# Kernel tuning notes

Hardware: AMD Instinct MI355X
Metric: run time of the kernel (lower is better)

Reference implementation:

```python
import jax, jax.numpy as jnp
import numpy as np

B, CIN, COUT, CLEV = 1, 128, 128, 64
H, W = 48, 160            # height//2**scale, width//2**scale (scale=2)
MIN_D, MAX_D = 0.1, 100.0


def conv3x3(x, w, b, mode):
    x = jnp.pad(x, ((0, 0), (0, 0), (1, 1), (1, 1)), mode=mode)
    y = jax.lax.conv_general_dilated(x, w, (1, 1), 'VALID',
                                     dimension_numbers=('NCHW', 'OIHW', 'NCHW'))
    return y + b[None, :, None, None]


def head(x, w1, b1, w2, b2):  # gaussian head: conv -> GELU -> conv, replicate pad
    return conv3x3(jax.nn.gelu(conv3x3(x, w1, b1, 'edge')), w2, b2, 'edge')


def convblock(x, w, b):  # ConvBlock: 3x3 conv (reflect pad) + ELU
    return jax.nn.elu(conv3x3(x, w, b, 'reflect'))


def to_pts(t):  # [B,C,H,W] -> [B,HW,C]
    return t.transpose(0, 2, 3, 1).reshape(t.shape[0], -1, t.shape[1])


def quat_to_rot(q):  # [N,4] (w,x,y,z) -> [N,3,3]
    w, x, y, z = q[:, 0], q[:, 1], q[:, 2], q[:, 3]
    return jnp.stack([1 - 2 * (y * y + z * z), 2 * (x * y - w * z), 2 * (x * z + w * y),
                      2 * (x * y + w * z), 1 - 2 * (x * x + z * z), 2 * (y * z - w * x),
                      2 * (x * z - w * y), 2 * (y * z + w * x), 1 - 2 * (x * x + y * y)],
                     axis=-1).reshape(-1, 3, 3)


def rasterize_one(pos, rot, scl, opa, feat, K):
    # depth-sort gaussians front-to-back
    order = jnp.argsort(pos[:, 2])
    pos, rot, scl, opa, feat = pos[order], rot[order], scl[order], opa[order], feat[order]
    x, y, z = pos[:, 0], pos[:, 1], pos[:, 2]
    fx, fy, cx, cy = K[0, 0], K[1, 1], K[0, 2], K[1, 2]
    u, v = fx * x / z + cx, fy * y / z + cy
    # 3D covariance Sigma = R S S^T R^T, projected with perspective Jacobian J
    M = quat_to_rot(rot) * scl[:, None, :]
    Sig = jnp.einsum('nij,nkj->nik', M, M)
    zer = jnp.zeros_like(z)
    J = jnp.stack([fx / z, zer, -fx * x / z ** 2,
                   zer, fy / z, -fy * y / z ** 2], axis=-1).reshape(-1, 2, 3)
    cov = jnp.einsum('nij,njk,nlk->nil', J, Sig, J)
    a = cov[:, 0, 0] + 0.3  # low-pass blur as in 3DGS
    bq = cov[:, 0, 1]
    c = cov[:, 1, 1] + 0.3
    det = a * c - bq * bq
    A, Bc, C = c / det, -bq / det, a / det  # conic (inverse 2D covariance)
    gy, gx = jnp.meshgrid(jnp.arange(H, dtype=pos.dtype),
                          jnp.arange(W, dtype=pos.dtype), indexing='ij')
    dx = gx.reshape(-1)[:, None] - u[None, :]  # [P,N]
    dy = gy.reshape(-1)[:, None] - v[None, :]
    power = -0.5 * (A[None] * dx * dx + C[None] * dy * dy) - Bc[None] * dx * dy
    alpha = jnp.where(power <= 0.,
                      jnp.clip(opa[None, :, 0] * jnp.exp(jnp.minimum(power, 0.)), 0., 0.99),
                      0.)
    l1m = jnp.log1p(-alpha)
    logT = jnp.cumsum(l1m, axis=1) - l1m  # exclusive transmittance along sorted axis
    wgt = alpha * jnp.exp(logT)           # [P,N]
    return (wgt @ feat).T.reshape(-1, H, W)  # [C,H,W]


def forward(init_feature, disp_init, inv_K, K,
            rot_w1, rot_b1, rot_w2, rot_b2,
            scl_w1, scl_b1, scl_w2, scl_b2,
            opa_w1, opa_b1, opa_w2, opa_b2,
            fl_w1, fl_b1, fl_w2, fl_b2, fr_w, fr_b):
    bs = init_feature.shape[0]
    # disp_to_depth
    scaled = 1. / MAX_D + (1. / MIN_D - 1. / MAX_D) * disp_init
    depth = jnp.clip(1. / scaled, MIN_D, MAX_D)
    # backproject depth to a point cloud
    gy, gx = jnp.meshgrid(jnp.arange(H, dtype=depth.dtype),
                          jnp.arange(W, dtype=depth.dtype), indexing='ij')
    pix = jnp.stack([gx.ravel(), gy.ravel(), jnp.ones(H * W, depth.dtype)], 0)  # [3,HW]
    cam = jnp.einsum('bij,jn->bin', inv_K[:, :3, :3], pix) * depth.reshape(bs, 1, -1)
    position = cam.transpose(0, 2, 1)  # [B,N,3]
    rot = head(init_feature, rot_w1, rot_b1, rot_w2, rot_b2)
    rot = rot / jnp.maximum(jnp.linalg.norm(rot, axis=1, keepdims=True), 1e-12)
    rotation = to_pts(rot)  # [B,N,4]
    scale = to_pts(jnp.abs(head(init_feature, scl_w1, scl_b1, scl_w2, scl_b2)))
    opacity = to_pts(jax.nn.sigmoid(head(init_feature, opa_w1, opa_b1, opa_w2, opa_b2)))
    gs_feat = to_pts(convblock(convblock(init_feature, fl_w1, fl_b1), fl_w2, fl_b2))
    lev = jax.vmap(rasterize_one)(position, rotation, scale, opacity, gs_feat, K)
    return convblock(lev, fr_w, fr_b)


def setup_inputs() -> dict:
    key = jax.random.key(0)
    ks = jax.random.split(key, 16)
    p = lambda i, shape: jax.random.normal(ks[i], shape, jnp.float32) * 0.05
    Kmat = np.array([[0.58 * W, 0, 0.5 * W, 0],
                     [0, 1.92 * H, 0.5 * H, 0],
                     [0, 0, 1, 0],
                     [0, 0, 0, 1]], dtype=np.float32)
    inv_K = np.linalg.inv(Kmat)
    return {
        'init_feature': jax.random.normal(ks[0], (B, CIN, H, W), jnp.float32),
        'disp_init': jax.random.uniform(ks[1], (B, 1, H, W), jnp.float32, 0.01, 0.99),
        'inv_K': jnp.tile(jnp.asarray(inv_K)[None], (B, 1, 1)),
        'K': jnp.tile(jnp.asarray(Kmat)[None], (B, 1, 1)),
        'rot_w1': p(2, (8, CIN, 3, 3)), 'rot_b1': jnp.zeros(8),
        'rot_w2': p(3, (4, 8, 3, 3)), 'rot_b2': jnp.zeros(4),
        'scl_w1': p(4, (6, CIN, 3, 3)), 'scl_b1': jnp.zeros(6),
        'scl_w2': p(5, (3, 6, 3, 3)), 'scl_b2': jnp.zeros(3),
        'opa_w1': p(6, (2, CIN, 3, 3)), 'opa_b1': jnp.zeros(2),
        'opa_w2': p(7, (1, 2, 3, 3)), 'opa_b2': jnp.zeros(1),
        'fl_w1': p(8, (CIN, CIN, 3, 3)), 'fl_b1': jnp.zeros(CIN),
        'fl_w2': p(9, (CLEV, CIN, 3, 3)), 'fl_b2': jnp.zeros(CLEV),
        'fr_w': p(10, (COUT, CLEV, 3, 3)), 'fr_b': jnp.zeros(COUT),
    }


def reference(init_feature, disp_init, inv_K, K, rot_w1, rot_b1, rot_w2, rot_b2,
              scl_w1, scl_b1, scl_w2, scl_b2, opa_w1, opa_b1, opa_w2, opa_b2,
              fl_w1, fl_b1, fl_w2, fl_b2, fr_w, fr_b):
    return forward(init_feature, disp_init, inv_K, K, rot_w1, rot_b1, rot_w2, rot_b2,
                   scl_w1, scl_b1, scl_w2, scl_b2, opa_w1, opa_b1, opa_w2, opa_b2,
                   fl_w1, fl_b1, fl_w2, fl_b2, fr_w, fr_b)
```

## Files before the change

kernel.cpp:

```cpp
#include <hip/hip_runtime.h>
#include <hip/hip_bf16.h>
#include <math.h>

#define Hh 48
#define Ww 160
#define NP 7680

using bf16 = __hip_bfloat16;
typedef __attribute__((ext_vector_type(8))) short v8s;
typedef __attribute__((ext_vector_type(4))) float v4f;

__device__ __forceinline__ float bfdec(unsigned short u) {
  return __uint_as_float(((unsigned)u) << 16);
}
__device__ __forceinline__ unsigned short bfenc(float x) {
  bf16 b = __float2bfloat16(x);
  return *(unsigned short*)&b;
}
__device__ __forceinline__ float ldany(const void* p, size_t i, int isbf) {
  return isbf ? bfdec(((const unsigned short*)p)[i]) : ((const float*)p)[i];
}

__device__ __forceinline__ int mapidx(int i, int n, int mode) {
  if (mode == 0) return i < 0 ? 0 : (i >= n ? n - 1 : i);
  return i < 0 ? -i : (i >= n ? 2 * n - 2 - i : i);
}

__device__ __forceinline__ float eluf(float v) { return v > 0.f ? v : expm1f(v); }
__device__ __forceinline__ float geluf(float v) {
  float c = v + 0.044715f * v * v * v;
  return 0.5f * v * (1.f + tanhf(0.7978845608028654f * c));
}

__global__ __launch_bounds__(256) void sniff_k(const unsigned short* __restrict__ w,
                                               int* __restrict__ flag) {
  __shared__ int cnt[256];
  int c = 0;
  for (int i = threadIdx.x; i < 2048; i += 256) {
    float a = fabsf(bfdec(w[i]));
    if (a > 1e-3f && a < 0.5f) c++;
  }
  cnt[threadIdx.x] = c;
  __syncthreads();
  for (int s = 128; s > 0; s >>= 1) {
    if (threadIdx.x < s) cnt[threadIdx.x] += cnt[threadIdx.x + s];
    __syncthreads();
  }
  if (threadIdx.x == 0) flag[0] = (cnt[0] > 1536) ? 1 : 0;
}

__global__ __launch_bounds__(256) void transpose_x_k(const int* __restrict__ flag,
    const void* __restrict__ xsrc, unsigned short* __restrict__ xb) {
  __shared__ float tile[32][33];
  const int f = *flag;
  const int pb = blockIdx.x * 32, cb = blockIdx.y * 32;
#pragma unroll
  for (int pass = 0; pass < 4; pass++) {
    int ci = (threadIdx.x >> 5) + pass * 8, pl = threadIdx.x & 31;
    tile[ci][pl] = ldany(xsrc, (size_t)(cb + ci) * NP + pb + pl, f);
  }
  __syncthreads();
#pragma unroll
  for (int pass = 0; pass < 4; pass++) {
    int pl = (threadIdx.x >> 5) + pass * 8, ci = threadIdx.x & 31;
    xb[(size_t)(pb + pl) * 128 + cb + ci] = bfenc(tile[ci][pl]);
  }
}

__global__ __launch_bounds__(256) void prep_k(const int* __restrict__ flag,
    const void* disp, const void* invK, const void* K, const void* rw2,
    const void* rb2, const void* sw2, const void* sb2, const void* ow2, const void* ob2,
    const void* rb1, const void* sb1, const void* ob1, const void* fb1, const void* fb2,
    const void* frb, const void* rot_w1, const void* scl_w1, const void* opa_w1,
    const void* fl_w1, const void* fl_w2, const void* fr_w,
    float* __restrict__ dispf, float* __restrict__ smallf, float* __restrict__ biasf,
    unsigned short* __restrict__ a_h1, unsigned short* __restrict__ a_fl1,
    unsigned short* __restrict__ a_fl2, unsigned short* __restrict__ a_fr, int permfr) {
  int i = blockIdx.x * 256 + threadIdx.x;
  int f = *flag;
  if (i < 7680) { dispf[i] = ldany(disp, i, f); return; }
  i -= 7680;
  if (i < 508) {
    const void* src; int off;
    if (i < 16)       { src = invK; off = i; }
    else if (i < 32)  { src = K;    off = i - 16; }
    else if (i < 320) { src = rw2;  off = i - 32; }
    else if (i < 324) { src = rb2;  off = i - 320; }
    else if (i < 486) { src = sw2;  off = i - 324; }
    else if (i < 489) { src = sb2;  off = i - 486; }
    else if (i < 507) { src = ow2;  off = i - 489; }
    else              { src = ob2;  off = i - 507; }
    smallf[i] = ldany(src, off, f); return;
  }
  i -= 508;
  if (i < 336) {
    if (i < 8) biasf[i] = ldany(rb1, i, f);
    else if (i < 14) biasf[i] = ldany(sb1, i - 8, f);
    else if (i < 16) biasf[i] = ldany(ob1, i - 14, f);
    else if (i < 144) biasf[i] = ldany(fb1, i - 16, f);
    else if (i < 208) biasf[i] = ldany(fb2, i - 144, f);
    else biasf[i] = ldany(frb, i - 208, f);
    return;
  }
  i -= 336;
  if (i < 73728) {
    int co = i / 1152, rem = i - co * 1152;
    int t = rem >> 7, ci = rem & 127;
    float v = 0.f;
    if (co < 8) v = ldany(rot_w1, (size_t)co * 1152 + ci * 9 + t, f);
    else if (co < 14) v = ldany(scl_w1, (size_t)(co - 8) * 1152 + ci * 9 + t, f);
    else if (co < 16) v = ldany(opa_w1, (size_t)(co - 14) * 1152 + ci * 9 + t, f);
    a_h1[i] = bfenc(v); return;
  }
  i -= 73728;
  if (i < 147456) {
    int co = i / 1152, rem = i - co * 1152;
    int t = rem >> 7, ci = rem & 127;
    a_fl1[i] = bfenc(ldany(fl_w1, (size_t)co * 1152 + ci * 9 + t, f)); return;
  }
  i -= 147456;
  if (i < 73728) {
    int co = i / 1152, rem = i - co * 1152;
    int t = rem >> 7, ci = rem & 127;
    a_fl2[i] = bfenc(ldany(fl_w2, (size_t)co * 1152 + ci * 9 + t, f)); return;
  }
  i -= 73728;
  if (i < 73728) {
    if (permfr) {
      int co = i / 576, rem = i - co * 576;
      int t = rem >> 6, ci = rem & 63;
      a_fr[i] = bfenc(ldany(fr_w, (size_t)co * 576 + ci * 9 + t, f));
    } else {
      a_fr[i] = bfenc(ldany(fr_w, i, f));
    }
    return;
  }
}

template<int OM, int PM, int ACT, bool GUARD, int KP, bool OPX>
__global__ __launch_bounds__(256) void gemm_conv4_k(const unsigned short* __restrict__ A,
    const unsigned short* __restrict__ X, const float* __restrict__ bias,
    void* __restrict__ out, const int* __restrict__ flag, int K, int glim) {
  __shared__ v8s As4[64][5];
  __shared__ v8s Bs4[64][5];
  __shared__ int off9s[64][9];
  const int tid = threadIdx.x;
  const int pxB = blockIdx.x * 64;
  const int coB = blockIdx.y * 64;
  if (tid < 64) {
    int p = pxB + tid;
    int h = p / Ww, w = p - h * Ww;
#pragma unroll
    for (int r = 0; r < 3; r++) {
      int hh = mapidx(h + r - 1, Hh, PM);
#pragma unroll
      for (int s = 0; s < 3; s++)
        off9s[tid][r * 3 + s] = hh * Ww + mapidx(w + s - 1, Ww, PM);
    }
  }
  const int lane = tid & 63, wv = tid >> 6;
  const int m16 = lane & 15, quad = lane >> 4;
  const int srow = tid >> 2, sg = tid & 3;
  v4f acc[4];
#pragma unroll
  for (int b = 0; b < 4; b++) acc[b] = (v4f){0.f, 0.f, 0.f, 0.f};
  __syncthreads();
  const int nIter = K >> 5;
  for (int it = 0; it < nIter; it++) {
    const int k0 = it << 5;
    {
      const unsigned short* ap = &A[(size_t)(coB + srow) * K + k0 + sg * 8];
      v8s av;
#pragma unroll
      for (int j = 0; j < 8; j++) av[j] = (short)ap[j];
      As4[srow][sg] = av;
    }
    {
      v8s bv;
      if (KP == 128) {
        int kk = k0 + sg * 8;
        int t = kk >> 7, c0 = kk & 127;
        const unsigned short* xp = &X[(size_t)off9s[srow][t] * 128 + c0];
#pragma unroll
        for (int j = 0; j < 8; j++) bv[j] = (short)xp[j];
      } else if (KP == 64) {
        int kk = k0 + sg * 8;
        int t = kk >> 6, c0 = kk & 63;
        const unsigned short* xp = &X[(size_t)off9s[srow][t] * 64 + c0];
#pragma unroll
        for (int j = 0; j < 8; j++) bv[j] = (short)xp[j];
      } else {
#pragma unroll
        for (int j = 0; j < 8; j++) {
          int k = k0 + sg * 8 + j;
          int ci = k / 9;
          int t = k - ci * 9;
          bv[j] = (short)X[(size_t)ci * NP + off9s[srow][t]];
        }
      }
      Bs4[srow][sg] = bv;
    }
    __syncthreads();
    v8s af = As4[wv * 16 + m16][quad];
    v8s bfr[4];
#pragma unroll
    for (int b = 0; b < 4; b++) bfr[b] = Bs4[b * 16 + m16][quad];
#pragma unroll
    for (int b = 0; b < 4; b++)
      acc[b] = __builtin_amdgcn_mfma_f32_16x16x32_bf16(af, bfr[b], acc[b], 0, 0, 0);
    __syncthreads();
  }
  const int obf = (OM == 2) ? *flag : (OM == 1);
#pragma unroll
  for (int b = 0; b < 4; b++) {
#pragma unroll
    for (int r = 0; r < 4; r++) {
      int co = coB + wv * 16 + quad * 4 + r;
      int px = pxB + b * 16 + m16;
      if (GUARD && co >= glim) continue;
      float bv = bias[GUARD ? (co & 15) : co];
      float v = acc[b][r] + bv;
      v = (ACT == 2) ? geluf(v) : eluf(v);
      size_t oi = OPX ? ((size_t)px * 128 + co) : ((size_t)co * NP + px);
      if (obf) ((unsigned short*)out)[oi] = bfenc(v);
      else ((float*)out)[oi] = v;
    }
  }
}

__global__ __launch_bounds__(256) void conv_fused1_k(
    const unsigned short* __restrict__ a_fl1, const unsigned short* __restrict__ a_h1,
    const unsigned short* __restrict__ X, const float* __restrict__ biasf,
    unsigned short* __restrict__ t1b, float* __restrict__ h1) {
  __shared__ v8s As4[64][5];
  __shared__ v8s Bs4[64][5];
  __shared__ int off9s[64][9];
  const int tid = threadIdx.x;
  const int zy = blockIdx.y;
  const bool ishead = (zy == 2);
  const int pm = ishead ? 0 : 1;
  const int pxB = blockIdx.x * 64;
  const int coB = ishead ? 0 : zy * 64;
  const unsigned short* A = ishead ? a_h1 : a_fl1;
  if (tid < 64) {
    int p = pxB + tid;
    int h = p / Ww, w = p - h * Ww;
#pragma unroll
    for (int r = 0; r < 3; r++) {
      int hh = mapidx(h + r - 1, Hh, pm);
#pragma unroll
      for (int s = 0; s < 3; s++)
        off9s[tid][r * 3 + s] = hh * Ww + mapidx(w + s - 1, Ww, pm);
    }
  }
  const int lane = tid & 63, wv = tid >> 6;
  const int m16 = lane & 15, quad = lane >> 4;
  const int srow = tid >> 2, sg = tid & 3;
  v4f acc[4];
#pragma unroll
  for (int b = 0; b < 4; b++) acc[b] = (v4f){0.f, 0.f, 0.f, 0.f};
  __syncthreads();
  for (int it = 0; it < 36; it++) {
    const int k0 = it << 5;
    {
      const unsigned short* ap = &A[(size_t)(coB + srow) * 1152 + k0 + sg * 8];
      v8s av;
#pragma unroll
      for (int j = 0; j < 8; j++) av[j] = (short)ap[j];
      As4[srow][sg] = av;
    }
    {
      int kk = k0 + sg * 8;
      int t = kk >> 7, c0 = kk & 127;
      const unsigned short* xp = &X[(size_t)off9s[srow][t] * 128 + c0];
      v8s bv;
#pragma unroll
      for (int j = 0; j < 8; j++) bv[j] = (short)xp[j];
      Bs4[srow][sg] = bv;
    }
    __syncthreads();
    v8s af = As4[wv * 16 + m16][quad];
    v8s bfr[4];
#pragma unroll
    for (int b = 0; b < 4; b++) bfr[b] = Bs4[b * 16 + m16][quad];
#pragma unroll
    for (int b = 0; b < 4; b++)
      acc[b] = __builtin_amdgcn_mfma_f32_16x16x32_bf16(af, bfr[b], acc[b], 0, 0, 0);
    __syncthreads();
  }
#pragma unroll
  for (int b = 0; b < 4; b++) {
#pragma unroll
    for (int r = 0; r < 4; r++) {
      int co = coB + wv * 16 + quad * 4 + r;
      int px = pxB + b * 16 + m16;
      if (ishead) {
        if (co < 16) h1[(size_t)co * NP + px] = geluf(acc[b][r] + biasf[co]);
      } else {
        t1b[(size_t)px * 128 + co] = bfenc(eluf(acc[b][r] + biasf[16 + co]));
      }
    }
  }
}

__global__ __launch_bounds__(64) void head2_prep_k(const float* __restrict__ h1,
    const float* __restrict__ smallf, const float* __restrict__ dispf,
    float* __restrict__ params, float* __restrict__ zbuf, int* __restrict__ rank) {
  const float* invK = smallf;
  const float* Km   = smallf + 16;
  const float* rw2  = smallf + 32;
  const float* rb2  = smallf + 320;
  const float* sw2  = smallf + 324;
  const float* sb2  = smallf + 486;
  const float* ow2  = smallf + 489;
  const float* ob2  = smallf + 507;
  int p = blockIdx.x * 64 + threadIdx.x;
  if (p >= NP) return;
  int hh = p / Ww, ww = p - hh * Ww;
  float racc[4], sacc[3], oacc;
#pragma unroll
  for (int i = 0; i < 4; i++) racc[i] = rb2[i];
#pragma unroll
  for (int i = 0; i < 3; i++) sacc[i] = sb2[i];
  oacc = ob2[0];
  for (int ci = 0; ci < 16; ci++) {
    float t9[9];
#pragma unroll
    for (int r = 0; r < 3; r++) {
      int rr = mapidx(hh + r - 1, Hh, 0);
#pragma unroll
      for (int s = 0; s < 3; s++) {
        int cc = mapidx(ww + s - 1, Ww, 0);
        t9[r * 3 + s] = h1[(size_t)ci * NP + rr * Ww + cc];
      }
    }
    if (ci < 8) {
      for (int co = 0; co < 4; co++)
#pragma unroll
        for (int k = 0; k < 9; k++)
          racc[co] = fmaf(t9[k], rw2[(co * 8 + ci) * 9 + k], racc[co]);
    } else if (ci < 14) {
      int c2 = ci - 8;
      for (int co = 0; co < 3; co++)
#pragma unroll
        for (int k = 0; k < 9; k++)
          sacc[co] = fmaf(t9[k], sw2[(co * 6 + c2) * 9 + k], sacc[co]);
    } else {
      int c2 = ci - 14;
#pragma unroll
      for (int k = 0; k < 9; k++)
        oacc = fmaf(t9[k], ow2[c2 * 9 + k], oacc);
    }
  }
  float nq = sqrtf(racc[0]*racc[0] + racc[1]*racc[1] + racc[2]*racc[2] + racc[3]*racc[3]);
  nq = fmaxf(nq, 1e-12f);
  float qw = racc[0] / nq, qx = racc[1] / nq, qy = racc[2] / nq, qz = racc[3] / nq;
  float s0 = fabsf(sacc[0]), s1 = fabsf(sacc[1]), s2 = fabsf(sacc[2]);
  float opa = 1.f / (1.f + __expf(-oacc));
  float d = dispf[p];
  float scaled = 0.01f + 9.99f * d;
  float depth = fminf(fmaxf(1.f / scaled, 0.1f), 100.f);
  float M00 = invK[0], M01 = invK[1], M02 = invK[2];
  float M10 = invK[4], M11 = invK[5], M12 = invK[6];
  float M20 = invK[8], M21 = invK[9], M22 = invK[10];
  float gxf = (float)ww, gyf = (float)hh;
  float X = (M00 * gxf + M01 * gyf + M02) * depth;
  float Y = (M10 * gxf + M11 * gyf + M12) * depth;
  float Z = (M20 * gxf + M21 * gyf + M22) * depth;
  float fxk = Km[0], fyk = Km[5];
  float cxk = Km[2], cyk = Km[6];
  float u = fxk * X / Z + cxk;
  float v = fyk * Y / Z + cyk;
  float R00 = 1.f - 2.f*(qy*qy + qz*qz), R01 = 2.f*(qx*qy - qw*qz), R02 = 2.f*(qx*qz + qw*qy);
  float R10 = 2.f*(qx*qy + qw*qz), R11 = 1.f - 2.f*(qx*qx + qz*qz), R12 = 2.f*(qy*qz - qw*qx);
  float R20 = 2.f*(qx*qz - qw*qy), R21 = 2.f*(qy*qz + qw*qx), R22 = 1.f - 2.f*(qx*qx + qy*qy);
  float M0a = R00*s0, M0b = R01*s1, M0c = R02*s2;
  float M1a = R10*s0, M1b = R11*s1, M1c = R12*s2;
  float M2a = R20*s0, M2b = R21*s1, M2c = R22*s2;
  float S00 = M0a*M0a + M0b*M0b + M0c*M0c;
  float S01 = M0a*M1a + M0b*M1b + M0c*M1c;
  float S02 = M0a*M2a + M0b*M2b + M0c*M2c;
  float S11 = M1a*M1a + M1b*M1b + M1c*M1c;
  float S12 = M1a*M2a + M1b*M2b + M1c*M2c;
  float S22 = M2a*M2a + M2b*M2b + M2c*M2c;
  float iz = 1.f / Z;
  float j00 = fxk * iz, j02 = -fxk * X * iz * iz;
  float j11 = fyk * iz, j12 = -fyk * Y * iz * iz;
  float c00 = j00*j00*S00 + 2.f*j00*j02*S02 + j02*j02*S22 + 0.3f;
  float c01 = j00*j11*S01 + j00*j12*S02 + j02*j11*S12 + j02*j12*S22;
  float c11 = j11*j11*S11 + 2.f*j11*j12*S12 + j12*j12*S22 + 0.3f;
  float det = c00 * c11 - c01 * c01;
  float idet = 1.f / det;
  float* pr = params + (size_t)p * 8;
  pr[0] = u; pr[1] = v; pr[2] = c11 * idet; pr[3] = -c01 * idet;
  pr[4] = c00 * idet; pr[5] = opa; pr[6] = Z; pr[7] = 0.f;
  zbuf[p] = Z;
  rank[p] = 0;
}

__global__ __launch_bounds__(256) void rank_count_k(const float* __restrict__ zbuf,
                                                    int* __restrict__ rank) {
  int i = blockIdx.x * 256 + threadIdx.x;
  int sid = blockIdx.y;
  float zi = zbuf[i];
  const float4* zv = (const float4*)(zbuf + sid * 960);
  int cnt = 0;
  for (int t = 0; t < 240; t++) {
    float4 z4 = zv[t];
    int jb = sid * 960 + t * 4;
    cnt += (z4.x < zi || (z4.x == zi && jb + 0 < i)) ? 1 : 0;
    cnt += (z4.y < zi || (z4.y == zi && jb + 1 < i)) ? 1 : 0;
    cnt += (z4.z < zi || (z4.z == zi && jb + 2 < i)) ? 1 : 0;
    cnt += (z4.w < zi || (z4.w == zi && jb + 3 < i)) ? 1 : 0;
  }
  atomicAdd(&rank[i], cnt);
}

__global__ __launch_bounds__(256) void scatter_k(const int* __restrict__ rank,
                                                 int* __restrict__ ord) {
  int i = blockIdx.x * 256 + threadIdx.x;
  ord[rank[i]] = i;
}

__global__ __launch_bounds__(256) void gather_all_k(const int* __restrict__ ord,
    const float* __restrict__ t2e, const float* __restrict__ params,
    unsigned short* __restrict__ featT, float* __restrict__ params_s) {
  int gid = blockIdx.x * 256 + threadIdx.x;
  if (gid < NP * 64) {
    int c = gid / NP, n = gid - c * NP;
    featT[gid] = bfenc(t2e[(size_t)c * NP + ord[n]]);
  } else {
    int g2 = gid - NP * 64;
    int n = g2 >> 3, c = g2 & 7;
    params_s[g2] = params[((size_t)ord[n] << 3) + c];
  }
}

__global__ __launch_bounds__(64) void raster_seq_k(const float* __restrict__ params_s,
    const unsigned short* __restrict__ featT, unsigned short* __restrict__ levb) {
  __shared__ unsigned int Wl[64][17];
  const int lane = threadIdx.x;
  const int m16 = lane & 15, quad = lane >> 4;
  const int pxB = blockIdx.x * 64;
  const int mypx = pxB + lane;
  const float px = (float)(mypx % Ww), py = (float)(mypx / Ww);
  float T = 1.f;
  v4f acc[4][4];
#pragma unroll
  for (int a = 0; a < 4; a++)
#pragma unroll
    for (int b = 0; b < 4; b++) acc[a][b] = (v4f){0.f, 0.f, 0.f, 0.f};
  const float4* pv = (const float4*)params_s;
  for (int sub = 0; sub < NP / 32; sub++) {
    const int g0 = sub * 32;
    float al[32];
#pragma unroll
    for (int j = 0; j < 32; j++) {
      float4 pa = pv[(g0 + j) * 2], pb = pv[(g0 + j) * 2 + 1];
      float dx = px - pa.x, dy = py - pa.y;
      float power = -0.5f * (pa.z * dx * dx + pb.x * dy * dy) - pa.w * dx * dy;
      al[j] = fminf(pb.y * __expf(power), 0.99f);
    }
#pragma unroll
    for (int jj = 0; jj < 16; jj++) {
      float w0 = al[2 * jj] * T;     T *= 1.f - al[2 * jj];
      float w1 = al[2 * jj + 1] * T; T *= 1.f - al[2 * jj + 1];
      Wl[lane][jj] = (unsigned)bfenc(w0) | ((unsigned)bfenc(w1) << 16);
    }
    v8s af[4], bfr[4];
#pragma unroll
    for (int a = 0; a < 4; a++) {
      unsigned d0 = Wl[a * 16 + m16][quad * 4 + 0];
      unsigned d1 = Wl[a * 16 + m16][quad * 4 + 1];
      unsigned d2 = Wl[a * 16 + m16][quad * 4 + 2];
      unsigned d3 = Wl[a * 16 + m16][quad * 4 + 3];
      v8s t;
      t[0] = (short)(d0 & 0xffff); t[1] = (short)(d0 >> 16);
      t[2] = (short)(d1 & 0xffff); t[3] = (short)(d1 >> 16);
      t[4] = (short)(d2 & 0xffff); t[5] = (short)(d2 >> 16);
      t[6] = (short)(d3 & 0xffff); t[7] = (short)(d3 >> 16);
      af[a] = t;
    }
#pragma unroll
    for (int b = 0; b < 4; b++) {
      const unsigned short* fp = &featT[(size_t)(b * 16 + m16) * NP + g0 + quad * 8];
      v8s t;
#pragma unroll
      for (int j = 0; j < 8; j++) t[j] = (short)fp[j];
      bfr[b] = t;
    }
#pragma unroll
    for (int a = 0; a < 4; a++)
#pragma unroll
      for (int b = 0; b < 4; b++)
        acc[a][b] = __builtin_amdgcn_mfma_f32_16x16x32_bf16(af[a], bfr[b], acc[a][b], 0, 0, 0);
    if (__all(T < 1e-7f)) break;
  }
#pragma unroll
  for (int a = 0; a < 4; a++) {
#pragma unroll
    for (int b = 0; b < 4; b++) {
#pragma unroll
      for (int r = 0; r < 4; r++) {
        levb[(size_t)(pxB + a * 16 + quad * 4 + r) * 64 + b * 16 + m16] =
            bfenc(acc[a][b][r]);
      }
    }
  }
}

extern "C" void kernel_launch(void* const* d_in, const int* in_sizes, int n_in,
                              void* d_out, int out_size, void* d_ws, size_t ws_size,
                              hipStream_t stream) {
  (void)in_sizes; (void)n_in; (void)out_size; (void)ws_size;
  const void* init_feature = d_in[0];
  const void* disp   = d_in[1];
  const void* invK   = d_in[2];
  const void* Km     = d_in[3];
  const void* rot_w1 = d_in[4];
  const void* rot_b1 = d_in[5];
  const void* rot_w2 = d_in[6];
  const void* rot_b2 = d_in[7];
  const void* scl_w1 = d_in[8];
  const void* scl_b1 = d_in[9];
  const void* scl_w2 = d_in[10];
  const void* scl_b2 = d_in[11];
  const void* opa_w1 = d_in[12];
  const void* opa_b1 = d_in[13];
  const void* opa_w2 = d_in[14];
  const void* opa_b2 = d_in[15];
  const void* fl_w1  = d_in[16];
  const void* fl_b1  = d_in[17];
  const void* fl_w2  = d_in[18];
  const void* fl_b2  = d_in[19];
  const void* fr_w   = d_in[20];
  const void* fr_b   = d_in[21];

  float* wsf = (float*)d_ws;
  int*   flag    = (int*)wsf;
  float* smallf  = wsf + 16;
  float* dispf   = wsf + 528;
  float* biasf   = wsf + 8208;
  unsigned short* a_h1  = (unsigned short*)(wsf + 8720);
  unsigned short* a_fl1 = (unsigned short*)(wsf + 45584);
  unsigned short* a_fl2 = (unsigned short*)(wsf + 119312);
  unsigned short* a_fr  = (unsigned short*)(wsf + 156176);
  unsigned short* xb    = (unsigned short*)(wsf + 193040);
  unsigned short* t1b   = (unsigned short*)(wsf + 684560);
  float* t2e     = wsf + 1176080;
  float* h1      = wsf + 1667600;
  float* params  = wsf + 1790480;
  float* params_s= wsf + 1851920;
  float* featbuf = wsf + 1913360;
  unsigned short* levb = (unsigned short*)(wsf + 2896400);
  float* zbuf    = wsf + 3142160;
  int*   rank    = (int*)(wsf + 3149840);
  int*   ord     = (int*)(wsf + 3157520);

  sniff_k<<<1, 256, 0, stream>>>((const unsigned short*)fl_w1, flag);
  transpose_x_k<<<dim3(240, 4), 256, 0, stream>>>(flag, init_feature, xb);
  prep_k<<<1474, 256, 0, stream>>>(flag,
      disp, invK, Km, rot_w2, rot_b2, scl_w2, scl_b2, opa_w2, opa_b2,
      rot_b1, scl_b1, opa_b1, fl_b1, fl_b2, fr_b,
      rot_w1, scl_w1, opa_w1, fl_w1, fl_w2, fr_w,
      dispf, smallf, biasf, a_h1, a_fl1, a_fl2, a_fr, 1);

  conv_fused1_k<<<dim3(120, 3), 256, 0, stream>>>(a_fl1, a_h1, xb, biasf, t1b, h1);
  gemm_conv4_k<0, 1, 1, false, 128, false><<<dim3(120, 1), 256, 0, stream>>>(
      a_fl2, t1b, biasf + 144, t2e, flag, 1152, 64);
  head2_prep_k<<<120, 64, 0, stream>>>(h1, smallf, dispf, params, zbuf, rank);
  rank_count_k<<<dim3(30, 8), 256, 0, stream>>>(zbuf, rank);
  scatter_k<<<30, 256, 0, stream>>>(rank, ord);

  gather_all_k<<<(NP * 72) / 256, 256, 0, stream>>>(ord, t2e, params,
      (unsigned short*)featbuf, params_s);
  raster_seq_k<<<120, 64, 0, stream>>>(params_s, (const unsigned short*)featbuf, levb);
  gemm_conv4_k<2, 1, 1, false, 64, false><<<dim3(120, 2), 256, 0, stream>>>(
      a_fr, levb, biasf + 208, d_out, flag, 576, 128);
}
```

Before: 222.3 us.

## Fold gather into rasterizer via indirect reads and merge prep kernels

The separate gather kernel that reordered features and Gaussian params by depth order is removed. The rasterizer now reads the sort order into shared memory and indexes params and a bf16 feature buffer indirectly. The second conv writes bf16 output directly (OM=1) instead of fp32. The input transpose kernel is merged into the prep kernel to save a launch. This trades one gather pass and a launch for scattered, uncoalesced feature loads and extra barriers inside the latency-bound sequential raster loop, which runs only 120 single-wave blocks.

```diff
diff --git a/kernel.cpp b/kernel.cpp
--- a/kernel.cpp
+++ b/kernel.cpp
@@ -49,25 +49,8 @@
   if (threadIdx.x == 0) flag[0] = (cnt[0] > 1536) ? 1 : 0;
 }
 
-__global__ __launch_bounds__(256) void transpose_x_k(const int* __restrict__ flag,
-    const void* __restrict__ xsrc, unsigned short* __restrict__ xb) {
-  __shared__ float tile[32][33];
-  const int f = *flag;
-  const int pb = blockIdx.x * 32, cb = blockIdx.y * 32;
-#pragma unroll
-  for (int pass = 0; pass < 4; pass++) {
-    int ci = (threadIdx.x >> 5) + pass * 8, pl = threadIdx.x & 31;
-    tile[ci][pl] = ldany(xsrc, (size_t)(cb + ci) * NP + pb + pl, f);
-  }
-  __syncthreads();
-#pragma unroll
-  for (int pass = 0; pass < 4; pass++) {
-    int pl = (threadIdx.x >> 5) + pass * 8, ci = threadIdx.x & 31;
-    xb[(size_t)(pb + pl) * 128 + cb + ci] = bfenc(tile[ci][pl]);
-  }
-}
-
-__global__ __launch_bounds__(256) void prep_k(const int* __restrict__ flag,
+__global__ __launch_bounds__(256) void prep_all_k(const int* __restrict__ flag,
+    const void* __restrict__ xsrc, unsigned short* __restrict__ xb,
     const void* disp, const void* invK, const void* K, const void* rw2,
     const void* rb2, const void* sw2, const void* sb2, const void* ow2, const void* ob2,
     const void* rb1, const void* sb1, const void* ob1, const void* fb1, const void* fb2,
@@ -75,9 +58,26 @@
     const void* fl_w1, const void* fl_w2, const void* fr_w,
     float* __restrict__ dispf, float* __restrict__ smallf, float* __restrict__ biasf,
     unsigned short* __restrict__ a_h1, unsigned short* __restrict__ a_fl1,
-    unsigned short* __restrict__ a_fl2, unsigned short* __restrict__ a_fr, int permfr) {
-  int i = blockIdx.x * 256 + threadIdx.x;
-  int f = *flag;
+    unsigned short* __restrict__ a_fl2, unsigned short* __restrict__ a_fr) {
+  __shared__ float tile[32][33];
+  const int f = *flag;
+  if (blockIdx.x < 960) {
+    const int bx = blockIdx.x;
+    const int pb = (bx % 240) * 32, cb = (bx / 240) * 32;
+#pragma unroll
+    for (int pass = 0; pass < 4; pass++) {
+      int ci = (threadIdx.x >> 5) + pass * 8, pl = threadIdx.x & 31;
+      tile[ci][pl] = ldany(xsrc, (size_t)(cb + ci) * NP + pb + pl, f);
+    }
+    __syncthreads();
+#pragma unroll
+    for (int pass = 0; pass < 4; pass++) {
+      int pl = (threadIdx.x >> 5) + pass * 8, ci = threadIdx.x & 31;
+      xb[(size_t)(pb + pl) * 128 + cb + ci] = bfenc(tile[ci][pl]);
+    }
+    return;
+  }
+  int i = (blockIdx.x - 960) * 256 + threadIdx.x;
   if (i < 7680) { dispf[i] = ldany(disp, i, f); return; }
   i -= 7680;
   if (i < 508) {
@@ -126,13 +126,9 @@
   }
   i -= 73728;
   if (i < 73728) {
-    if (permfr) {
-      int co = i / 576, rem = i - co * 576;
-      int t = rem >> 6, ci = rem & 63;
-      a_fr[i] = bfenc(ldany(fr_w, (size_t)co * 576 + ci * 9 + t, f));
-    } else {
-      a_fr[i] = bfenc(ldany(fr_w, i, f));
-    }
+    int co = i / 576, rem = i - co * 576;
+    int t = rem >> 6, ci = rem & 63;
+    a_fr[i] = bfenc(ldany(fr_w, (size_t)co * 576 + ci * 9 + t, f));
     return;
   }
 }
@@ -422,23 +418,11 @@
   ord[rank[i]] = i;
 }
 
-__global__ __launch_bounds__(256) void gather_all_k(const int* __restrict__ ord,
-    const float* __restrict__ t2e, const float* __restrict__ params,
-    unsigned short* __restrict__ featT, float* __restrict__ params_s) {
-  int gid = blockIdx.x * 256 + threadIdx.x;
-  if (gid < NP * 64) {
-    int c = gid / NP, n = gid - c * NP;
-    featT[gid] = bfenc(t2e[(size_t)c * NP + ord[n]]);
-  } else {
-    int g2 = gid - NP * 64;
-    int n = g2 >> 3, c = g2 & 7;
-    params_s[g2] = params[((size_t)ord[n] << 3) + c];
-  }
-}
-
-__global__ __launch_bounds__(64) void raster_seq_k(const float* __restrict__ params_s,
-    const unsigned short* __restrict__ featT, unsigned short* __restrict__ levb) {
+__global__ __launch_bounds__(64) void raster_seq_k(const int* __restrict__ ord,
+    const float* __restrict__ params, const unsigned short* __restrict__ t2eb,
+    unsigned short* __restrict__ levb) {
   __shared__ unsigned int Wl[64][17];
+  __shared__ int ords[32];
   const int lane = threadIdx.x;
   const int m16 = lane & 15, quad = lane >> 4;
   const int pxB = blockIdx.x * 64;
@@ -450,13 +434,19 @@
   for (int a = 0; a < 4; a++)
 #pragma unroll
     for (int b = 0; b < 4; b++) acc[a][b] = (v4f){0.f, 0.f, 0.f, 0.f};
-  const float4* pv = (const float4*)params_s;
   for (int sub = 0; sub < NP / 32; sub++) {
     const int g0 = sub * 32;
+    if (lane < 32) ords[lane] = ord[g0 + lane];
+    __syncthreads();
+    int myord[8];
+#pragma unroll
+    for (int j = 0; j < 8; j++) myord[j] = ords[quad * 8 + j];
     float al[32];
 #pragma unroll
     for (int j = 0; j < 32; j++) {
-      float4 pa = pv[(g0 + j) * 2], pb = pv[(g0 + j) * 2 + 1];
+      const float* pp = params + ((size_t)ords[j] << 3);
+      float4 pa = *(const float4*)pp;
+      float4 pb = *(const float4*)(pp + 4);
       float dx = px - pa.x, dy = py - pa.y;
       float power = -0.5f * (pa.z * dx * dx + pb.x * dy * dy) - pa.w * dx * dy;
       al[j] = fminf(pb.y * __expf(power), 0.99f);
@@ -483,10 +473,10 @@
     }
 #pragma unroll
     for (int b = 0; b < 4; b++) {
-      const unsigned short* fp = &featT[(size_t)(b * 16 + m16) * NP + g0 + quad * 8];
+      const unsigned short* fp = &t2eb[(size_t)(b * 16 + m16) * NP];
       v8s t;
 #pragma unroll
-      for (int j = 0; j < 8; j++) t[j] = (short)fp[j];
+      for (int j = 0; j < 8; j++) t[j] = (short)fp[myord[j]];
       bfr[b] = t;
     }
 #pragma unroll
@@ -495,6 +485,7 @@
       for (int b = 0; b < 4; b++)
         acc[a][b] = __builtin_amdgcn_mfma_f32_16x16x32_bf16(af[a], bfr[b], acc[a][b], 0, 0, 0);
     if (__all(T < 1e-7f)) break;
+    __syncthreads();
   }
 #pragma unroll
   for (int a = 0; a < 4; a++) {
@@ -547,34 +538,29 @@
   unsigned short* a_fr  = (unsigned short*)(wsf + 156176);
   unsigned short* xb    = (unsigned short*)(wsf + 193040);
   unsigned short* t1b   = (unsigned short*)(wsf + 684560);
-  float* t2e     = wsf + 1176080;
+  unsigned short* t2eb  = (unsigned short*)(wsf + 1176080);
   float* h1      = wsf + 1667600;
   float* params  = wsf + 1790480;
-  float* params_s= wsf + 1851920;
-  float* featbuf = wsf + 1913360;
   unsigned short* levb = (unsigned short*)(wsf + 2896400);
   float* zbuf    = wsf + 3142160;
   int*   rank    = (int*)(wsf + 3149840);
   int*   ord     = (int*)(wsf + 3157520);
 
   sniff_k<<<1, 256, 0, stream>>>((const unsigned short*)fl_w1, flag);
-  transpose_x_k<<<dim3(240, 4), 256, 0, stream>>>(flag, init_feature, xb);
-  prep_k<<<1474, 256, 0, stream>>>(flag,
+  prep_all_k<<<2434, 256, 0, stream>>>(flag, init_feature, xb,
       disp, invK, Km, rot_w2, rot_b2, scl_w2, scl_b2, opa_w2, opa_b2,
       rot_b1, scl_b1, opa_b1, fl_b1, fl_b2, fr_b,
       rot_w1, scl_w1, opa_w1, fl_w1, fl_w2, fr_w,
-      dispf, smallf, biasf, a_h1, a_fl1, a_fl2, a_fr, 1);
+      dispf, smallf, biasf, a_h1, a_fl1, a_fl2, a_fr);
 
   conv_fused1_k<<<dim3(120, 3), 256, 0, stream>>>(a_fl1, a_h1, xb, biasf, t1b, h1);
-  gemm_conv4_k<0, 1, 1, false, 128, false><<<dim3(120, 1), 256, 0, stream>>>(
-      a_fl2, t1b, biasf + 144, t2e, flag, 1152, 64);
+  gemm_conv4_k<1, 1, 1, false, 128, false><<<dim3(120, 1), 256, 0, stream>>>(
+      a_fl2, t1b, biasf + 144, t2eb, flag, 1152, 64);
   head2_prep_k<<<120, 64, 0, stream>>>(h1, smallf, dispf, params, zbuf, rank);
   rank_count_k<<<dim3(30, 8), 256, 0, stream>>>(zbuf, rank);
   scatter_k<<<30, 256, 0, stream>>>(rank, ord);
 
-  gather_all_k<<<(NP * 72) / 256, 256, 0, stream>>>(ord, t2e, params,
-      (unsigned short*)featbuf, params_s);
-  raster_seq_k<<<120, 64, 0, stream>>>(params_s, (const unsigned short*)featbuf, levb);
+  raster_seq_k<<<120, 64, 0, stream>>>(ord, params, t2eb, levb);
   gemm_conv4_k<2, 1, 1, false, 64, false><<<dim3(120, 2), 256, 0, stream>>>(
       a_fr, levb, biasf + 208, d_out, flag, 576, 128);
 }
```

Measured after the change: 224.9 us. About the same (+1.2%).
